# Kernel optimization log

Hardware: AMD Instinct MI355X
Metric: run time of the kernel (lower is better)

## Reference

```python
import jax, jax.numpy as jnp
import numpy as np

K = 20
NEG = 0.2      # leaky relu slope
EPS = 1e-5     # layernorm eps


def knn(x, k=K):
    # x: [B, C, N] -> neighbor indices [B, N, k] by largest negative sq-distance
    xt = jnp.swapaxes(x, 1, 2)                      # [B, N, C]
    inner = -2.0 * jnp.einsum('bnc,bcm->bnm', xt, x)
    xx = jnp.sum(x * x, axis=1)                     # [B, N]
    pd = -xx[:, :, None] - inner - xx[:, None, :]   # [B, N, N]
    _, idx = jax.lax.top_k(pd, k)
    return idx


def graph_feature(x, k=K):
    # x: [B, C, N] -> edge features [B, 2C, N, k] = cat(neighbor - center, center)
    xt = jnp.swapaxes(x, 1, 2)                      # [B, N, C]
    idx = knn(x, k)                                 # [B, N, k]
    nbr = jax.vmap(lambda f, i: f[i])(xt, idx)      # [B, N, k, C]
    ctr = jnp.broadcast_to(xt[:, :, None, :], nbr.shape)
    feat = jnp.concatenate([nbr - ctr, ctr], axis=-1)
    return jnp.transpose(feat, (0, 3, 1, 2))


def lrelu(x):
    return jnp.where(x >= 0, x, NEG * x)


def conv1x1(x, w):
    # x: [B, C, N, k], w: [O, C]  (BatchNorm2d in eval with default stats == identity)
    return jnp.einsum('oc,bcnk->bonk', w, x)


def layernorm(x, g, b):
    m = jnp.mean(x, axis=-1, keepdims=True)
    v = jnp.var(x, axis=-1, keepdims=True)
    return (x - m) * jax.lax.rsqrt(v + EPS) * g + b


def l2n(x):
    return x / jnp.linalg.norm(x, axis=1, keepdims=True)


def fc_layer(x, w, bias, g, beta):
    # l2-normalize -> Linear -> LayerNorm -> LeakyReLU (fc_layer with norm=True, bn=True)
    x = l2n(x)
    x = x @ w.T
    if bias is not None:
        x = x + bias
    return lrelu(layernorm(x, g, beta))


def transform_net(f0, tw1, tw2, tw3, tfc1_w, tfc1_g, tfc1_b, tfc2_w, tfc2_bias, tfc2_g, tfc2_b, tfc3_w, tfc3_b):
    # f0: [B, 6, N, k]
    h = lrelu(conv1x1(f0, tw1))                     # [B, 64, N, k]
    h = lrelu(conv1x1(h, tw2))                      # [B, 128, N, k]
    h = jnp.max(h, axis=-1, keepdims=True)          # [B, 128, N, 1]
    h = lrelu(conv1x1(h, tw3))                      # [B, 1024, N, 1]
    h = jnp.max(h, axis=2)[:, :, 0]                 # [B, 1024]
    h = fc_layer(h, tfc1_w, None, tfc1_g, tfc1_b)   # dgcnn: fc1 bias=False
    h = fc_layer(h, tfc2_w, tfc2_bias, tfc2_g, tfc2_b)
    h = h @ tfc3_w.T + tfc3_b                       # [B, 9]
    h = h + jnp.eye(3, dtype=h.dtype).reshape(9)
    return h.reshape(-1, 3, 3)


def setup_inputs() -> dict:
    key = jax.random.key(0)
    ks = jax.random.split(key, 16)

    def w(k, o, i):
        return jax.random.normal(k, (o, i), dtype=jnp.float32) / np.sqrt(i)

    inp = {
        'x': jax.random.normal(ks[0], (16, 3, 1024), dtype=jnp.float32),
        # transform_net params
        'tw1': w(ks[1], 64, 6),
        'tw2': w(ks[2], 128, 64),
        'tw3': w(ks[3], 1024, 128),
        'tfc1_w': w(ks[4], 512, 1024),
        'tfc1_g': jnp.ones((512,), jnp.float32),
        'tfc1_b': jnp.zeros((512,), jnp.float32),
        'tfc2_w': w(ks[5], 256, 512),
        'tfc2_bias': jnp.zeros((256,), jnp.float32),
        'tfc2_g': jnp.ones((256,), jnp.float32),
        'tfc2_b': jnp.zeros((256,), jnp.float32),
        'tfc3_w': w(ks[6], 9, 256) * 0.01,
        'tfc3_b': jnp.zeros((9,), jnp.float32),
        # EdgeConv params (1x1 convs, bias=False for dgcnn)
        'w1': w(ks[7], 64, 6),
        'w2': w(ks[8], 64, 128),
        'w3': w(ks[9], 128, 128),
        'w4': w(ks[10], 256, 256),
        'w5': w(ks[11], 1024, 512),
    }
    return inp


def reference(x, tw1, tw2, tw3, tfc1_w, tfc1_g, tfc1_b, tfc2_w, tfc2_bias, tfc2_g, tfc2_b,
              tfc3_w, tfc3_b, w1, w2, w3, w4, w5):
    # spatial transform from first graph feature
    f0 = graph_feature(x)                           # [B, 6, N, k]
    t = transform_net(f0, tw1, tw2, tw3, tfc1_w, tfc1_g, tfc1_b,
                      tfc2_w, tfc2_bias, tfc2_g, tfc2_b, tfc3_w, tfc3_b)
    x = jnp.einsum('bij,bjn->bin', t, x)            # [B, 3, N]

    # 4 EdgeConv blocks: graph_feature -> 1x1 conv (+BN identity) -> lrelu -> max over k
    x1 = jnp.max(lrelu(conv1x1(graph_feature(x), w1)), axis=-1)    # [B, 64, N]
    x2 = jnp.max(lrelu(conv1x1(graph_feature(x1), w2)), axis=-1)   # [B, 64, N]
    x3 = jnp.max(lrelu(conv1x1(graph_feature(x2), w3)), axis=-1)   # [B, 128, N]
    x4 = jnp.max(lrelu(conv1x1(graph_feature(x3), w4)), axis=-1)   # [B, 256, N]

    xc = jnp.concatenate([x1, x2, x3, x4], axis=1)  # [B, 512, N]
    x5 = lrelu(jnp.einsum('oc,bcn->bon', w5, xc))   # [B, 1024, N]
    return jnp.max(x5, axis=-1)                     # [B, 1024] global feature
```

## Files before the change

kernel.cpp:

```cpp
#include <hip/hip_runtime.h>
#include <math.h>

#define BATCH 16
#define NPTS 1024
#define KNN 20

__device__ __forceinline__ float lrelu(float v) { return v >= 0.f ? v : 0.2f * v; }

typedef __attribute__((ext_vector_type(8))) short bf16x8;
typedef __attribute__((ext_vector_type(4))) float f32x4;
typedef unsigned long long ull;

__device__ __forceinline__ ushort f2bf(float f) {
  union { float f; unsigned u; } v; v.f = f;
  unsigned r = (v.u + 0x7FFFu + ((v.u >> 16) & 1u)) >> 16;
  return (ushort)r;
}

__device__ __forceinline__ unsigned wave_min_u32(unsigned v) {
  unsigned t;
  t = (unsigned)__builtin_amdgcn_update_dpp((int)v, (int)v, 0x111, 0xf, 0xf, false);
  v = t < v ? t : v;
  t = (unsigned)__builtin_amdgcn_update_dpp((int)v, (int)v, 0x112, 0xf, 0xf, false);
  v = t < v ? t : v;
  t = (unsigned)__builtin_amdgcn_update_dpp((int)v, (int)v, 0x114, 0xf, 0xf, false);
  v = t < v ? t : v;
  t = (unsigned)__builtin_amdgcn_update_dpp((int)v, (int)v, 0x118, 0xf, 0xf, false);
  v = t < v ? t : v;
  t = (unsigned)__builtin_amdgcn_update_dpp((int)v, (int)v, 0x142, 0xf, 0xf, false);
  v = t < v ? t : v;
  t = (unsigned)__builtin_amdgcn_update_dpp((int)v, (int)v, 0x143, 0xf, 0xf, false);
  v = t < v ? t : v;
  return (unsigned)__builtin_amdgcn_readlane((int)v, 63);
}

__global__ __launch_bounds__(256)
void wsplit_t_kernel(const float* __restrict__ W, float* __restrict__ waT,
                     float* __restrict__ wdT, int O, int Cc) {
  int e = blockIdx.x * 256 + threadIdx.x;
  if (e < O * Cc) {
    int c = e / O, o = e - c * O;
    float a = W[o * 2 * Cc + c], bb = W[o * 2 * Cc + Cc + c];
    waT[e] = a; wdT[e] = bb - a;
  }
}

__global__ __launch_bounds__(256)
void wsplit_bf_kernel(const float* __restrict__ W, ushort* __restrict__ wa_bf,
                      ushort* __restrict__ wd_bf, int O, int Cc) {
  int e = blockIdx.x * 256 + threadIdx.x;
  if (e < O * Cc) {
    int o = e / Cc, c = e - o * Cc;
    float a = W[o * 2 * Cc + c], bb = W[o * 2 * Cc + Cc + c];
    wa_bf[e] = f2bf(a); wd_bf[e] = f2bf(bb - a);
  }
}

__global__ __launch_bounds__(256)
void cvt_bf16_kernel(const float* __restrict__ in, ushort* __restrict__ outp, int n) {
  int e = blockIdx.x * 256 + threadIdx.x;
  if (e < n) outp[e] = f2bf(in[e]);
}

__global__ __launch_bounds__(256)
void wtrans_kernel(const float* __restrict__ W, float* __restrict__ wT, int O, int Cc) {
  int e = blockIdx.x * 256 + threadIdx.x;
  if (e < O * Cc) {
    int c = e / O, o = e - c * O;
    wT[e] = W[(size_t)o * Cc + c];
  }
}

__global__ __launch_bounds__(256)
void xx3_kernel(const float* __restrict__ x, float* __restrict__ xx) {
  const int b = blockIdx.y;
  const int n = blockIdx.x * 256 + threadIdx.x;
  const float* xb = x + (size_t)b * 3 * NPTS;
  float a = xb[n], bb = xb[NPTS + n], c = xb[2 * NPTS + n];
  xx[b * NPTS + n] = a * a + bb * bb + c * c;
}

template<int C>
__global__ __launch_bounds__(256)
void knn_cn_kernel(const float* __restrict__ Xt, long sb,
                   const float* __restrict__ xx, int* __restrict__ idxout) {
  __shared__ float sc4[4][NPTS];
  const int b = blockIdx.y, i0 = blockIdx.x * 16;
  const int tid = threadIdx.x;
  const float* Xb = Xt + (size_t)b * sb;
  const int j0 = tid * 4;
  float acc[16][4];
  #pragma unroll
  for (int q = 0; q < 16; ++q)
    #pragma unroll
    for (int u = 0; u < 4; ++u) acc[q][u] = 0.f;
  for (int c = 0; c < C; ++c) {
    const float4 xv = *reinterpret_cast<const float4*>(Xb + (size_t)c * NPTS + j0);
    const float* xr = Xb + (size_t)c * NPTS + i0;
    #pragma unroll
    for (int q = 0; q < 16; ++q) {
      const float xiq = xr[q];
      acc[q][0] = fmaf(xiq, xv.x, acc[q][0]);
      acc[q][1] = fmaf(xiq, xv.y, acc[q][1]);
      acc[q][2] = fmaf(xiq, xv.z, acc[q][2]);
      acc[q][3] = fmaf(xiq, xv.w, acc[q][3]);
    }
  }
  const float4 xxj = *reinterpret_cast<const float4*>(xx + b * NPTS + j0);
  const int wv = tid >> 6, lane = tid & 63;
  unsigned ku[4][16];

  #pragma unroll
  for (int r = 0; r < 4; ++r) {
    if (r > 0) __syncthreads();
    #pragma unroll
    for (int q = 0; q < 4; ++q) {
      const int qq = r * 4 + q;
      float4 st;
      st.x = fmaf(-2.f, acc[qq][0], xxj.x);
      st.y = fmaf(-2.f, acc[qq][1], xxj.y);
      st.z = fmaf(-2.f, acc[qq][2], xxj.z);
      st.w = fmaf(-2.f, acc[qq][3], xxj.w);
      *reinterpret_cast<float4*>(&sc4[q][j0]) = st;
    }
    __syncthreads();
    #pragma unroll
    for (int s = 0; s < 16; ++s) {
      const unsigned u = __float_as_uint(sc4[wv][lane + 64 * s]);
      ku[r][s] = u ^ ((unsigned)((int)u >> 31) | 0x80000000u);
    }
  }

  unsigned c1s[4], c2s[4]; int c1j[4], c2j[4];
  #pragma unroll
  for (int r = 0; r < 4; ++r) {
    unsigned b1 = 0xFFFFFFFFu, b2 = 0xFFFFFFFFu; int s1 = 0, s2 = 0;
    #pragma unroll
    for (int s = 0; s < 16; ++s) {
      const unsigned k = ku[r][s];
      const bool a1 = k < b1, a2 = k < b2;
      const unsigned n1 = a1 ? k : b1;  const int ns1 = a1 ? s : s1;
      const unsigned n2 = a1 ? b1 : (a2 ? k : b2);
      const int ns2 = a1 ? s1 : (a2 ? s : s2);
      b1 = n1; s1 = ns1; b2 = n2; s2 = ns2;
    }
    c1s[r] = b1; c1j[r] = lane + (s1 << 6);
    c2s[r] = b2; c2j[r] = lane + (s2 << 6);
  }
  const unsigned INVS = 0xFFFFFFFFu;
  int my[4] = {0, 0, 0, 0};
  for (int t = 0; t < KNN; ++t) {
    unsigned ws[4]; int wl[4], jw[4];
    #pragma unroll
    for (int r = 0; r < 4; ++r) ws[r] = wave_min_u32(c1s[r]);
    #pragma unroll
    for (int r = 0; r < 4; ++r) wl[r] = __ffsll((long long)__ballot(c1s[r] == ws[r])) - 1;
    #pragma unroll
    for (int r = 0; r < 4; ++r) jw[r] = __builtin_amdgcn_readlane(c1j[r], wl[r]);
    if (lane == t) {
      #pragma unroll
      for (int r = 0; r < 4; ++r) my[r] = jw[r];
    }
    bool cons = false;
    #pragma unroll
    for (int r = 0; r < 4; ++r) {
      const bool win = (lane == wl[r]);
      c1s[r] = win ? c2s[r] : c1s[r];
      c1j[r] = win ? c2j[r] : c1j[r];
      c2s[r] = win ? INVS : c2s[r];
      cons = cons || (c1s[r] == INVS);
    }
    if (__any(cons)) {
      #pragma unroll
      for (int r = 0; r < 4; ++r) {
        if (c1s[r] == INVS) {
          unsigned m1 = INVS, m2 = INVS; int r1 = 0, r2 = 0;
          #pragma unroll
          for (int s = 0; s < 16; ++s) {
            const unsigned k = ku[r][s];
            const bool ok = k > ws[r];
            const bool a1 = ok && (k < m1), a2 = ok && (k < m2);
            const unsigned nm1 = a1 ? k : m1;  const int nr1 = a1 ? s : r1;
            const unsigned nm2 = a1 ? m1 : (a2 ? k : m2);
            const int nr2 = a1 ? r1 : (a2 ? s : r2);
            m1 = nm1; r1 = nr1; m2 = nm2; r2 = nr2;
          }
          c1s[r] = (m1 == INVS) ? 0xFFFFFFFEu : m1;  c1j[r] = lane + (r1 << 6);
          c2s[r] = (m2 == INVS) ? 0xFFFFFFFEu : m2;  c2j[r] = lane + (r2 << 6);
        }
      }
    }
  }
  if (lane < KNN) {
    #pragma unroll
    for (int r = 0; r < 4; ++r)
      idxout[(size_t)(b * NPTS + i0 + r * 4 + wv) * KNN + lane] = my[r];
  }
}

__global__ __launch_bounds__(256)
void gemm_dual_kernel(const float* __restrict__ X, long sxb, int sxn, int sxc,
                      const float* __restrict__ WaT, const float* __restrict__ WdT,
                      int ldW, int C,
                      float* __restrict__ outY, float* __restrict__ outZ,
                      int sob, int son) {
  __shared__ __align__(16) float Xs[16][64];
  __shared__ __align__(16) float Was[16][64];
  __shared__ __align__(16) float Wds[16][64];
  const int b = blockIdx.z;
  const int n0 = blockIdx.x * 64, o0 = blockIdx.y * 64;
  const int tid = threadIdx.x;
  const int lr = tid & 63;
  const int c4 = (tid >> 6) * 4;
  const int tn = tid & 15, to = tid >> 4;
  float accY[4][4], accZ[4][4];
  #pragma unroll
  for (int i = 0; i < 4; ++i)
    #pragma unroll
    for (int j = 0; j < 4; ++j) { accY[i][j] = 0.f; accZ[i][j] = 0.f; }

  const size_t xbase = (size_t)b * sxb;
  for (int k0 = 0; k0 < C; k0 += 16) {
    #pragma unroll
    for (int u = 0; u < 4; ++u) {
      int c = k0 + c4 + u;
      float xv = 0.f, wa = 0.f, wd = 0.f;
      if (c < C) {
        xv = X[xbase + (size_t)(n0 + lr) * sxn + (size_t)c * sxc];
        wa = WaT[(size_t)c * ldW + o0 + lr];
        wd = WdT[(size_t)c * ldW + o0 + lr];
      }
      Xs[c4 + u][lr] = xv;
      Was[c4 + u][lr] = wa;
      Wds[c4 + u][lr] = wd;
    }
    __syncthreads();
    #pragma unroll
    for (int kk = 0; kk < 16; ++kk) {
      const float4 xa = *reinterpret_cast<const float4*>(&Xs[kk][tn * 4]);
      const float4 wav = *reinterpret_cast<const float4*>(&Was[kk][to * 4]);
      const float4 wdv = *reinterpret_cast<const float4*>(&Wds[kk][to * 4]);
      const float xr[4] = {xa.x, xa.y, xa.z, xa.w};
      const float war[4] = {wav.x, wav.y, wav.z, wav.w};
      const float wdr[4] = {wdv.x, wdv.y, wdv.z, wdv.w};
      #pragma unroll
      for (int i = 0; i < 4; ++i)
        #pragma unroll
        for (int j = 0; j < 4; ++j) {
          accY[i][j] = fmaf(xr[i], war[j], accY[i][j]);
          accZ[i][j] = fmaf(xr[i], wdr[j], accZ[i][j]);
        }
    }
    __syncthreads();
  }
  #pragma unroll
  for (int i = 0; i < 4; ++i) {
    const size_t base = (size_t)b * sob + (size_t)(n0 + tn * 4 + i) * son + o0 + to * 4;
    *reinterpret_cast<float4*>(&outY[base]) =
      make_float4(accY[i][0], accY[i][1], accY[i][2], accY[i][3]);
    *reinterpret_cast<float4*>(&outZ[base]) =
      make_float4(accZ[i][0], accZ[i][1], accZ[i][2], accZ[i][3]);
  }
}

template<int EPI>
__global__ __launch_bounds__(256)
void gemm128_kernel(const float* __restrict__ X, long sxb, int scN,
                    const float* __restrict__ WT, int ldW, int C,
                    float* __restrict__ out, int sob, int son, int snb) {
  __shared__ __align__(16) float Xs[16][128];
  __shared__ __align__(16) float Ws[16][128];
  __shared__ __align__(16) float red[16][132];
  const int b = blockIdx.z;
  const int n0 = blockIdx.x * 128, o0 = blockIdx.y * 128;
  const int tid = threadIdx.x;
  const int tn = tid & 15, to = tid >> 4;
  float acc[8][8];
  #pragma unroll
  for (int i = 0; i < 8; ++i)
    #pragma unroll
    for (int j = 0; j < 8; ++j) acc[i][j] = 0.f;

  const size_t xbase = (size_t)b * sxb;
  for (int c0 = 0; c0 < C; c0 += 16) {
    #pragma unroll
    for (int it = 0; it < 2; ++it) {
      const int task = tid + it * 256;
      const int kk = task >> 5, n4 = (task & 31) * 4;
      *reinterpret_cast<float4*>(&Xs[kk][n4]) =
        *reinterpret_cast<const float4*>(&X[xbase + (size_t)(c0 + kk) * scN + n0 + n4]);
      *reinterpret_cast<float4*>(&Ws[kk][n4]) =
        *reinterpret_cast<const float4*>(&WT[(size_t)(c0 + kk) * ldW + o0 + n4]);
    }
    __syncthreads();
    #pragma unroll
    for (int kk = 0; kk < 16; ++kk) {
      const float4 xa0 = *reinterpret_cast<const float4*>(&Xs[kk][tn * 4]);
      const float4 xa1 = *reinterpret_cast<const float4*>(&Xs[kk][64 + tn * 4]);
      const float4 wb0 = *reinterpret_cast<const float4*>(&Ws[kk][to * 4]);
      const float4 wb1 = *reinterpret_cast<const float4*>(&Ws[kk][64 + to * 4]);
      const float xr[8] = {xa0.x, xa0.y, xa0.z, xa0.w, xa1.x, xa1.y, xa1.z, xa1.w};
      const float wr[8] = {wb0.x, wb0.y, wb0.z, wb0.w, wb1.x, wb1.y, wb1.z, wb1.w};
      #pragma unroll
      for (int i = 0; i < 8; ++i)
        #pragma unroll
        for (int j = 0; j < 8; ++j) acc[i][j] = fmaf(xr[i], wr[j], acc[i][j]);
    }
    __syncthreads();
  }

  if (EPI == 0) {
    #pragma unroll
    for (int i = 0; i < 8; ++i) {
      const int n = n0 + (i >> 2) * 64 + tn * 4 + (i & 3);
      float4 s0 = make_float4(acc[i][0], acc[i][1], acc[i][2], acc[i][3]);
      float4 s1 = make_float4(acc[i][4], acc[i][5], acc[i][6], acc[i][7]);
      *reinterpret_cast<float4*>(&out[(size_t)b * sob + (size_t)n * son + o0 + to * 4]) = s0;
      *reinterpret_cast<float4*>(&out[(size_t)b * sob + (size_t)n * son + o0 + 64 + to * 4]) = s1;
    }
  } else {
    #pragma unroll
    for (int j = 0; j < 8; ++j) {
      float m = lrelu(acc[0][j]);
      #pragma unroll
      for (int i = 1; i < 8; ++i) m = fmaxf(m, lrelu(acc[i][j]));
      red[tn][(j >> 2) * 64 + to * 4 + (j & 3)] = m;
    }
    __syncthreads();
    if (tid < 128) {
      float m = red[0][tid];
      #pragma unroll
      for (int t = 1; t < 16; ++t) m = fmaxf(m, red[t][tid]);
      out[(size_t)b * sob + (size_t)blockIdx.x * snb + o0 + tid] = m;
    }
  }
}

template<int EPI>
__global__ __launch_bounds__(256)
void gemm_mfma_kernel(const ushort* __restrict__ Xg, long sxb, int ldX,
                      const ushort* __restrict__ Wg, int ldW, int K,
                      float* __restrict__ out, long sob, int son, int snb) {
  __shared__ __align__(16) ushort As[128 * 64];
  __shared__ __align__(16) ushort Bs[128 * 64];
  __shared__ float red[2][128];
  const int b = blockIdx.z;
  const int n0 = blockIdx.x * 128, o0 = blockIdx.y * 128;
  const int tid = threadIdx.x;
  const int lane = tid & 63;
  const int wrow = (tid >> 6) >> 1, wcol = (tid >> 6) & 1;
  f32x4 acc[4][4];
  #pragma unroll
  for (int i = 0; i < 4; ++i)
    #pragma unroll
    for (int j = 0; j < 4; ++j)
      #pragma unroll
      for (int r = 0; r < 4; ++r) acc[i][j][r] = 0.f;

  const ushort* Xb = Xg + (size_t)b * sxb;
  for (int kb = 0; kb < K; kb += 64) {
    #pragma unroll
    for (int i = 0; i < 4; ++i) {
      const int idx = i * 256 + tid;
      const int n = idx >> 3, kc = idx & 7;
      const bf16x8 xv = *reinterpret_cast<const bf16x8*>(&Xb[(size_t)(n0 + n) * ldX + kb + kc * 8]);
      const bf16x8 wv = *reinterpret_cast<const bf16x8*>(&Wg[(size_t)(o0 + n) * ldW + kb + kc * 8]);
      const int ad = n * 128 + ((kc * 16) ^ ((n & 7) << 4));
      *reinterpret_cast<bf16x8*>((char*)As + ad) = xv;
      *reinterpret_cast<bf16x8*>((char*)Bs + ad) = wv;
    }
    __syncthreads();
    #pragma unroll
    for (int s = 0; s < 2; ++s) {
      bf16x8 af[4], bfr[4];
      const int klane = (s * 64 + ((lane >> 4) << 4));
      #pragma unroll
      for (int f = 0; f < 4; ++f) {
        const int nl = wrow * 64 + f * 16 + (lane & 15);
        af[f] = *reinterpret_cast<const bf16x8*>((char*)As + nl * 128 + (klane ^ ((nl & 7) << 4)));
        const int ol = wcol * 64 + f * 16 + (lane & 15);
        bfr[f] = *reinterpret_cast<const bf16x8*>((char*)Bs + ol * 128 + (klane ^ ((ol & 7) << 4)));
      }
      #pragma unroll
      for (int i = 0; i < 4; ++i)
        #pragma unroll
        for (int j = 0; j < 4; ++j)
          acc[i][j] = __builtin_amdgcn_mfma_f32_16x16x32_bf16(af[i], bfr[j], acc[i][j], 0, 0, 0);
    }
    __syncthreads();
  }

  if (EPI == 0) {
    #pragma unroll
    for (int i = 0; i < 4; ++i)
      #pragma unroll
      for (int r = 0; r < 4; ++r) {
        const int n = n0 + wrow * 64 + i * 16 + ((lane >> 4) << 2) + r;
        #pragma unroll
        for (int j = 0; j < 4; ++j) {
          const int o = o0 + wcol * 64 + j * 16 + (lane & 15);
          out[(size_t)b * sob + (size_t)n * son + o] = acc[i][j][r];
        }
      }
  } else {
    #pragma unroll
    for (int j = 0; j < 4; ++j) {
      float m = -3.4e38f;
      #pragma unroll
      for (int i = 0; i < 4; ++i)
        #pragma unroll
        for (int r = 0; r < 4; ++r) m = fmaxf(m, lrelu(acc[i][j][r]));
      m = fmaxf(m, __shfl_xor(m, 16));
      m = fmaxf(m, __shfl_xor(m, 32));
      if (lane < 16) red[wrow][wcol * 64 + j * 16 + lane] = m;
    }
    __syncthreads();
    if (tid < 128) {
      float m = fmaxf(red[0][tid], red[1][tid]);
      out[(size_t)b * sob + (size_t)blockIdx.x * snb + o0 + tid] = m;
    }
  }
}

template<int O, int TI>
__global__ __launch_bounds__(256)
void edge_max_cn_kernel(const float* __restrict__ y, const float* __restrict__ z,
                        const int* __restrict__ idx, float* __restrict__ outCN,
                        float* __restrict__ xx, ushort* __restrict__ xbf, int choff) {
  __shared__ float tile[TI][O + 1];
  const int b = blockIdx.y;
  const int i0 = blockIdx.x * TI;
  const int wv = threadIdx.x >> 6, lane = threadIdx.x & 63;
  constexpr int OSEG = O / 64;
  constexpr int ROUNDS = TI * OSEG / 4;
  for (int r = 0; r < ROUNDS; ++r) {
    const int item = r * 4 + wv;
    const int il = item / OSEG, os = item - il * OSEG;
    const int i = i0 + il, o = os * 64 + lane;
    const int* ip = idx + (size_t)(b * NPTS + i) * KNN;
    const float zv = z[(size_t)(b * NPTS + i) * O + o];
    float m = -3.4e38f;
    #pragma unroll
    for (int t = 0; t < KNN; ++t) {
      int j = ip[t];
      float v = y[(size_t)(b * NPTS + j) * O + o] + zv;
      m = fmaxf(m, lrelu(v));
    }
    tile[il][o] = m;
    xbf[(size_t)(b * NPTS + i) * 512 + choff + o] = f2bf(m);
  }
  __syncthreads();
  if (xx != nullptr && threadIdx.x < TI) {
    const int il = threadIdx.x;
    float s = 0.f;
    #pragma unroll
    for (int o = 0; o < O; ++o) { float v = tile[il][o]; s = fmaf(v, v, s); }
    xx[b * NPTS + i0 + il] = s;
  }
  for (int e = threadIdx.x; e < TI * O; e += 256) {
    const int o = e / TI, il = e - o * TI;
    outCN[(size_t)b * 512 * NPTS + (size_t)o * NPTS + i0 + il] = tile[il][o];
  }
}

__global__ __launch_bounds__(256)
void h12_gemm_kernel(const float* __restrict__ ya, const float* __restrict__ zb,
                     const int* __restrict__ idx, const float* __restrict__ tw2T,
                     float* __restrict__ h2m) {
  __shared__ __align__(16) float h1s[80][68];
  __shared__ __align__(16) float ws[64][128];
  __shared__ __align__(16) float zbs[4][64];
  __shared__ float ot[128][4];
  __shared__ int idxs[4][KNN];
  const int b = blockIdx.y;
  const int i0 = blockIdx.x * 4;
  const int tid = threadIdx.x;

  #pragma unroll
  for (int it = 0; it < 8; ++it) {
    const int f = tid + it * 256;
    *reinterpret_cast<float4*>(&ws[0][0] + f * 4) =
      *reinterpret_cast<const float4*>(tw2T + (size_t)f * 4);
  }
  if (tid < 64) {
    const int p = tid >> 4, cq = (tid & 15) * 4;
    *reinterpret_cast<float4*>(&zbs[p][cq]) =
      *reinterpret_cast<const float4*>(&zb[(size_t)(b * NPTS + i0 + p) * 64 + cq]);
  }
  if (tid >= 64 && tid < 64 + 4 * KNN) {
    const int e = tid - 64;
    idxs[e / KNN][e % KNN] = idx[(size_t)(b * NPTS + i0) * KNN + e];
  }
  __syncthreads();

  #pragma unroll
  for (int it = 0; it < 5; ++it) {
    const int task = tid + it * 256;
    const int e = task >> 4, cq = (task & 15) * 4;
    const int p = e / KNN, t = e - p * KNN;
    const int j = idxs[p][t];
    const float4 yv = *reinterpret_cast<const float4*>(&ya[(size_t)(b * NPTS + j) * 64 + cq]);
    const float4 zv = *reinterpret_cast<const float4*>(&zbs[p][cq]);
    float4 hv;
    hv.x = lrelu(yv.x + zv.x); hv.y = lrelu(yv.y + zv.y);
    hv.z = lrelu(yv.z + zv.z); hv.w = lrelu(yv.w + zv.w);
    *reinterpret_cast<float4*>(&h1s[e][cq]) = hv;
  }
  __syncthreads();

  const int eg = tid >> 4, og = tid & 15;
  float acc[5][8];
  #pragma unroll
  for (int u = 0; u < 5; ++u)
    #pragma unroll
    for (int v = 0; v < 8; ++v) acc[u][v] = 0.f;
  #pragma unroll 4
  for (int kk = 0; kk < 64; ++kk) {
    float hv[5];
    #pragma unroll
    for (int u = 0; u < 5; ++u) hv[u] = h1s[eg * 5 + u][kk];
    const float4 w0 = *reinterpret_cast<const float4*>(&ws[kk][og * 4]);
    const float4 w1 = *reinterpret_cast<const float4*>(&ws[kk][64 + og * 4]);
    const float wr[8] = {w0.x, w0.y, w0.z, w0.w, w1.x, w1.y, w1.z, w1.w};
    #pragma unroll
    for (int u = 0; u < 5; ++u)
      #pragma unroll
      for (int v = 0; v < 8; ++v) acc[u][v] = fmaf(hv[u], wr[v], acc[u][v]);
  }

  const int p = eg >> 2, d = eg & 3;
  float m[8];
  #pragma unroll
  for (int v = 0; v < 8; ++v) {
    float mm = lrelu(acc[0][v]);
    #pragma unroll
    for (int u = 1; u < 5; ++u) mm = fmaxf(mm, lrelu(acc[u][v]));
    mm = fmaxf(mm, __shfl_xor(mm, 16));
    mm = fmaxf(mm, __shfl_xor(mm, 32));
    m[v] = mm;
  }
  if (d == 0) {
    #pragma unroll
    for (int v = 0; v < 8; ++v) {
      const int o = og * 4 + (v & 3) + (v >> 2) * 64;
      ot[o][p] = m[v];
    }
  }
  __syncthreads();
  if (tid < 128) {
    float4 st = make_float4(ot[tid][0], ot[tid][1], ot[tid][2], ot[tid][3]);
    *reinterpret_cast<float4*>(&h2m[(size_t)(b * 128 + tid) * NPTS + i0]) = st;
  }
}

__global__ __launch_bounds__(256)
void reduce_max_kernel(const float* __restrict__ part, float* __restrict__ outp, int nt) {
  const int b = blockIdx.y;
  const int o = blockIdx.x * 256 + threadIdx.x;
  float m = part[(size_t)(b * nt) * 1024 + o];
  for (int t = 1; t < nt; ++t) m = fmaxf(m, part[(size_t)(b * nt + t) * 1024 + o]);
  outp[b * 1024 + o] = m;
}

__device__ __forceinline__ float block_reduce_sum(float v, float* rbuf) {
  #pragma unroll
  for (int off = 32; off > 0; off >>= 1) v += __shfl_xor(v, off);
  const int w = threadIdx.x >> 6, lane = threadIdx.x & 63;
  const int nw = blockDim.x >> 6;
  if (lane == 0) rbuf[w] = v;
  __syncthreads();
  float tot = 0.f;
  for (int i = 0; i < nw; ++i) tot += rbuf[i];
  __syncthreads();
  return tot;
}

__global__ __launch_bounds__(256)
void fcall_kernel(const float* __restrict__ part,
                  const float* __restrict__ Wt1, const float* __restrict__ g1,
                  const float* __restrict__ bb1,
                  const float* __restrict__ Wt2, const float* __restrict__ bias2,
                  const float* __restrict__ g2, const float* __restrict__ bb2,
                  const float* __restrict__ Wt3, const float* __restrict__ bb3,
                  const float* __restrict__ x, float* __restrict__ xt) {
  __shared__ __align__(16) float gin[1024];
  __shared__ __align__(16) float f1s[512];
  __shared__ float f2s[256];
  __shared__ float hbuf[512];
  __shared__ float rbuf[8];
  __shared__ float tm[9];
  const int b = blockIdx.x, tid = threadIdx.x;
  for (int e = tid; e < 1024; e += 256) {
    const float* pp = part + (size_t)b * 8192 + e;
    float m = pp[0];
    #pragma unroll
    for (int t = 1; t < 8; ++t) m = fmaxf(m, pp[t * 1024]);
    gin[e] = m;
  }
  __syncthreads();
  float ps = 0.f;
  for (int e = tid; e < 1024; e += 256) ps = fmaf(gin[e], gin[e], ps);
  float ss = block_reduce_sum(ps, rbuf);
  float rinv = 1.0f / sqrtf(ss);
  #pragma unroll
  for (int r = 0; r < 2; ++r) {
    int o = tid + r * 256;
    const float* wrow = Wt1 + (size_t)o * 1024;
    float a = 0.f;
    for (int c4 = 0; c4 < 256; ++c4) {
      float4 wv = *reinterpret_cast<const float4*>(wrow + c4 * 4);
      float4 gv = *reinterpret_cast<const float4*>(&gin[c4 * 4]);
      a = fmaf(wv.x, gv.x, a); a = fmaf(wv.y, gv.y, a);
      a = fmaf(wv.z, gv.z, a); a = fmaf(wv.w, gv.w, a);
    }
    hbuf[o] = a * rinv;
  }
  __syncthreads();
  float pm = hbuf[tid] + hbuf[tid + 256];
  float mean = block_reduce_sum(pm, rbuf) * (1.f / 512.f);
  float d0 = hbuf[tid] - mean, d1 = hbuf[tid + 256] - mean;
  float var = block_reduce_sum(d0 * d0 + d1 * d1, rbuf) * (1.f / 512.f);
  float rs = 1.0f / sqrtf(var + 1e-5f);
  #pragma unroll
  for (int r = 0; r < 2; ++r) {
    int o = tid + r * 256;
    f1s[o] = lrelu((hbuf[o] - mean) * rs * g1[o] + bb1[o]);
  }
  __syncthreads();
  float ps2 = 0.f;
  for (int e = tid; e < 512; e += 256) ps2 = fmaf(f1s[e], f1s[e], ps2);
  float ss2 = block_reduce_sum(ps2, rbuf);
  float rinv2 = 1.0f / sqrtf(ss2);
  const float* wrow2 = Wt2 + (size_t)tid * 512;
  float a2 = 0.f;
  for (int c4 = 0; c4 < 128; ++c4) {
    float4 wv = *reinterpret_cast<const float4*>(wrow2 + c4 * 4);
    float4 gv = *reinterpret_cast<const float4*>(&f1s[c4 * 4]);
    a2 = fmaf(wv.x, gv.x, a2); a2 = fmaf(wv.y, gv.y, a2);
    a2 = fmaf(wv.z, gv.z, a2); a2 = fmaf(wv.w, gv.w, a2);
  }
  a2 = a2 * rinv2 + bias2[tid];
  float mean2 = block_reduce_sum(a2, rbuf) * (1.f / 256.f);
  float dd = a2 - mean2;
  float var2 = block_reduce_sum(dd * dd, rbuf) * (1.f / 256.f);
  float rs2 = 1.0f / sqrtf(var2 + 1e-5f);
  f2s[tid] = lrelu((a2 - mean2) * rs2 * g2[tid] + bb2[tid]);
  __syncthreads();
  if (tid < 9) {
    const float* wrow3 = Wt3 + tid * 256;
    float a3 = 0.f;
    for (int c = 0; c < 256; ++c) a3 = fmaf(wrow3[c], f2s[c], a3);
    a3 += bb3[tid];
    if (tid == 0 || tid == 4 || tid == 8) a3 += 1.f;
    tm[tid] = a3;
  }
  __syncthreads();
  const float* xb = x + (size_t)b * 3 * NPTS;
  float* ob = xt + (size_t)b * 3 * NPTS;
  #pragma unroll
  for (int nt = 0; nt < 4; ++nt) {
    const int n = nt * 256 + tid;
    const float x0 = xb[n], x1 = xb[NPTS + n], x2 = xb[2 * NPTS + n];
    #pragma unroll
    for (int i = 0; i < 3; ++i)
      ob[i * NPTS + n] = fmaf(tm[3 * i], x0, fmaf(tm[3 * i + 1], x1, tm[3 * i + 2] * x2));
  }
}

extern "C" void kernel_launch(void* const* d_in, const int* in_sizes, int n_in,
                              void* d_out, int out_size, void* d_ws, size_t ws_size,
                              hipStream_t stream) {
  (void)in_sizes; (void)n_in; (void)out_size; (void)ws_size;
  const float* x       = (const float*)d_in[0];
  const float* tw1     = (const float*)d_in[1];
  const float* tw2     = (const float*)d_in[2];
  const float* tw3     = (const float*)d_in[3];
  const float* tfc1_w  = (const float*)d_in[4];
  const float* tfc1_g  = (const float*)d_in[5];
  const float* tfc1_b  = (const float*)d_in[6];
  const float* tfc2_w  = (const float*)d_in[7];
  const float* tfc2_bias = (const float*)d_in[8];
  const float* tfc2_g  = (const float*)d_in[9];
  const float* tfc2_b  = (const float*)d_in[10];
  const float* tfc3_w  = (const float*)d_in[11];
  const float* tfc3_b  = (const float*)d_in[12];
  const float* w1      = (const float*)d_in[13];
  const float* w2      = (const float*)d_in[14];
  const float* w3      = (const float*)d_in[15];
  const float* w4      = (const float*)d_in[16];
  const float* w5      = (const float*)d_in[17];
  float* out = (float*)d_out;

  char* wsb = (char*)d_ws;
  size_t off = 0;
  auto alloc = [&](size_t bytes) -> void* {
    void* p = wsb + off;
    off += (bytes + 255) & ~(size_t)255;
    return p;
  };
  float* ybuf = (float*)alloc((size_t)BATCH * NPTS * 256 * 4);
  float* zbuf = (float*)alloc((size_t)BATCH * NPTS * 256 * 4);
  float* xcT  = (float*)alloc((size_t)BATCH * 512 * NPTS * 4);
  ushort* xc_bf = (ushort*)alloc((size_t)BATCH * NPTS * 512 * 2);
  float* h2m  = (float*)alloc((size_t)BATCH * 128 * NPTS * 4);
  float* part = (float*)alloc((size_t)BATCH * 16 * 1024 * 4);
  int*   idxb = (int*)alloc((size_t)BATCH * NPTS * KNN * 4);
  float* xxb  = (float*)alloc((size_t)BATCH * NPTS * 4);
  float* xt   = (float*)alloc((size_t)BATCH * 3 * NPTS * 4);
  float* tw1aT = (float*)alloc(3 * 64 * 4);
  float* tw1dT = (float*)alloc(3 * 64 * 4);
  float* w1aT  = (float*)alloc(3 * 64 * 4);
  float* w1dT  = (float*)alloc(3 * 64 * 4);
  float* w2aT  = (float*)alloc(64 * 64 * 4);
  float* w2dT  = (float*)alloc(64 * 64 * 4);
  float* w3aT  = (float*)alloc(64 * 128 * 4);
  float* w3dT  = (float*)alloc(64 * 128 * 4);
  ushort* w4a_bf = (ushort*)alloc(256 * 128 * 2);
  ushort* w4d_bf = (ushort*)alloc(256 * 128 * 2);
  ushort* w5_bf  = (ushort*)alloc(1024 * 512 * 2);
  float* tw2T  = (float*)alloc(64 * 128 * 4);
  float* tw3T  = (float*)alloc(128 * 1024 * 4);

  wsplit_t_kernel<<<1, 256, 0, stream>>>(tw1, tw1aT, tw1dT, 64, 3);
  wsplit_t_kernel<<<1, 256, 0, stream>>>(w1, w1aT, w1dT, 64, 3);
  wsplit_t_kernel<<<16, 256, 0, stream>>>(w2, w2aT, w2dT, 64, 64);
  wsplit_t_kernel<<<32, 256, 0, stream>>>(w3, w3aT, w3dT, 128, 64);
  wsplit_bf_kernel<<<128, 256, 0, stream>>>(w4, w4a_bf, w4d_bf, 256, 128);
  cvt_bf16_kernel<<<2048, 256, 0, stream>>>(w5, w5_bf, 1024 * 512);
  wtrans_kernel<<<32, 256, 0, stream>>>(tw2, tw2T, 128, 64);
  wtrans_kernel<<<512, 256, 0, stream>>>(tw3, tw3T, 1024, 128);

  xx3_kernel<<<dim3(4, 16), 256, 0, stream>>>(x, xxb);
  knn_cn_kernel<3><<<dim3(64, 16), 256, 0, stream>>>(x, 3 * NPTS, xxb, idxb);
  gemm_dual_kernel<<<dim3(16, 1, 16), 256, 0, stream>>>(x, 3 * NPTS, 1, NPTS, tw1aT, tw1dT,
                                                        64, 3, ybuf, zbuf, NPTS * 64, 64);
  h12_gemm_kernel<<<dim3(256, 16), 256, 0, stream>>>(ybuf, zbuf, idxb, tw2T, h2m);
  gemm128_kernel<1><<<dim3(8, 8, 16), 256, 0, stream>>>(h2m, 128 * NPTS, NPTS, tw3T, 1024, 128,
                                                        part, 8 * 1024, 0, 1024);
  fcall_kernel<<<16, 256, 0, stream>>>(part, tfc1_w, tfc1_g, tfc1_b,
                                       tfc2_w, tfc2_bias, tfc2_g, tfc2_b,
                                       tfc3_w, tfc3_b, x, xt);

  xx3_kernel<<<dim3(4, 16), 256, 0, stream>>>(xt, xxb);
  knn_cn_kernel<3><<<dim3(64, 16), 256, 0, stream>>>(xt, 3 * NPTS, xxb, idxb);
  gemm_dual_kernel<<<dim3(16, 1, 16), 256, 0, stream>>>(xt, 3 * NPTS, 1, NPTS, w1aT, w1dT,
                                                        64, 3, ybuf, zbuf, NPTS * 64, 64);
  edge_max_cn_kernel<64, 64><<<dim3(16, 16), 256, 0, stream>>>(ybuf, zbuf, idxb, xcT, xxb,
                                                               xc_bf, 0);

  knn_cn_kernel<64><<<dim3(64, 16), 256, 0, stream>>>(xcT, 512 * NPTS, xxb, idxb);
  gemm_dual_kernel<<<dim3(16, 1, 16), 256, 0, stream>>>(xcT, 512 * NPTS, 1, NPTS, w2aT, w2dT,
                                                        64, 64, ybuf, zbuf, NPTS * 64, 64);
  edge_max_cn_kernel<64, 64><<<dim3(16, 16), 256, 0, stream>>>(ybuf, zbuf, idxb,
                                                               xcT + 64 * NPTS, xxb, xc_bf, 64);

  knn_cn_kernel<64><<<dim3(64, 16), 256, 0, stream>>>(xcT + 64 * NPTS, 512 * NPTS, xxb, idxb);
  gemm_dual_kernel<<<dim3(16, 2, 16), 256, 0, stream>>>(xcT + 64 * NPTS, 512 * NPTS, 1, NPTS,
                                                        w3aT, w3dT, 128, 64,
                                                        ybuf, zbuf, NPTS * 128, 128);
  edge_max_cn_kernel<128, 64><<<dim3(16, 16), 256, 0, stream>>>(ybuf, zbuf, idxb,
                                                                xcT + 128 * NPTS, xxb, xc_bf, 128);

  knn_cn_kernel<128><<<dim3(64, 16), 256, 0, stream>>>(xcT + 128 * NPTS, 512 * NPTS, xxb, idxb);
  gemm_mfma_kernel<0><<<dim3(8, 2, 16), 256, 0, stream>>>(xc_bf + 128, (long)NPTS * 512, 512,
                                                          w4a_bf, 128, 128,
                                                          ybuf, (long)NPTS * 256, 256, 0);
  gemm_mfma_kernel<0><<<dim3(8, 2, 16), 256, 0, stream>>>(xc_bf + 128, (long)NPTS * 512, 512,
                                                          w4d_bf, 128, 128,
                                                          zbuf, (long)NPTS * 256, 256, 0);
  edge_max_cn_kernel<256, 32><<<dim3(32, 16), 256, 0, stream>>>(ybuf, zbuf, idxb,
                                                                xcT + 256 * NPTS, nullptr,
                                                                xc_bf, 256);

  gemm_mfma_kernel<1><<<dim3(8, 8, 16), 256, 0, stream>>>(xc_bf, (long)NPTS * 512, 512,
                                                          w5_bf, 512, 512,
                                                          part, 8 * 1024, 0, 1024);
  reduce_max_kernel<<<dim3(4, 16), 256, 0, stream>>>(part, out, 8);
}
```

Before: 734.9 us.

## Merge weight-prep kernels, split FC head into batched kernels, simplify knn argmin

Eight weight-preparation launches are folded into one flat-indexed prep kernel to cut launch overhead. The single per-batch FC head kernel, which streamed the full FC1/FC2 weight matrices once per batch, is split into three kernels. FC1 and FC2 now tile the weights in shared memory and reuse each tile across all 16 batches, and a final per-batch kernel does the last layernorm, the 3x3 transform and the point rotation. In the knn top-k loop, the ballot/ffs/readlane winner lookup is replaced by a second DPP wave-min over candidate indices, which changes tie-breaking to the smallest index. The FC split adds two launches and intermediate global buffers.

```diff
diff --git a/kernel.cpp b/kernel.cpp
--- a/kernel.cpp
+++ b/kernel.cpp
@@ -9,7 +9,6 @@
 
 typedef __attribute__((ext_vector_type(8))) short bf16x8;
 typedef __attribute__((ext_vector_type(4))) float f32x4;
-typedef unsigned long long ull;
 
 __device__ __forceinline__ ushort f2bf(float f) {
   union { float f; unsigned u; } v; v.f = f;
@@ -35,39 +34,56 @@
 }
 
 __global__ __launch_bounds__(256)
-void wsplit_t_kernel(const float* __restrict__ W, float* __restrict__ waT,
-                     float* __restrict__ wdT, int O, int Cc) {
-  int e = blockIdx.x * 256 + threadIdx.x;
-  if (e < O * Cc) {
-    int c = e / O, o = e - c * O;
-    float a = W[o * 2 * Cc + c], bb = W[o * 2 * Cc + Cc + c];
-    waT[e] = a; wdT[e] = bb - a;
-  }
-}
-
-__global__ __launch_bounds__(256)
-void wsplit_bf_kernel(const float* __restrict__ W, ushort* __restrict__ wa_bf,
-                      ushort* __restrict__ wd_bf, int O, int Cc) {
-  int e = blockIdx.x * 256 + threadIdx.x;
-  if (e < O * Cc) {
-    int o = e / Cc, c = e - o * Cc;
-    float a = W[o * 2 * Cc + c], bb = W[o * 2 * Cc + Cc + c];
-    wa_bf[e] = f2bf(a); wd_bf[e] = f2bf(bb - a);
-  }
-}
-
-__global__ __launch_bounds__(256)
-void cvt_bf16_kernel(const float* __restrict__ in, ushort* __restrict__ outp, int n) {
-  int e = blockIdx.x * 256 + threadIdx.x;
-  if (e < n) outp[e] = f2bf(in[e]);
-}
-
-__global__ __launch_bounds__(256)
-void wtrans_kernel(const float* __restrict__ W, float* __restrict__ wT, int O, int Cc) {
-  int e = blockIdx.x * 256 + threadIdx.x;
-  if (e < O * Cc) {
-    int c = e / O, o = e - c * O;
-    wT[e] = W[(size_t)o * Cc + c];
+void prep_all_kernel(const float* __restrict__ tw1, const float* __restrict__ w1,
+                     const float* __restrict__ w2, const float* __restrict__ w3,
+                     const float* __restrict__ w4, const float* __restrict__ w5,
+                     const float* __restrict__ tw2, const float* __restrict__ tw3,
+                     float* __restrict__ tw1aT, float* __restrict__ tw1dT,
+                     float* __restrict__ w1aT, float* __restrict__ w1dT,
+                     float* __restrict__ w2aT, float* __restrict__ w2dT,
+                     float* __restrict__ w3aT, float* __restrict__ w3dT,
+                     ushort* __restrict__ w4a_bf, ushort* __restrict__ w4d_bf,
+                     ushort* __restrict__ w5_bf,
+                     float* __restrict__ tw2T, float* __restrict__ tw3T) {
+  int g = blockIdx.x * 256 + threadIdx.x;
+  if (g < 524288) { w5_bf[g] = f2bf(w5[g]); return; }
+  g -= 524288;
+  if (g < 131072) { int c = g >> 10, o = g & 1023; tw3T[g] = tw3[o * 128 + c]; return; }
+  g -= 131072;
+  if (g < 32768) {
+    int o = g >> 7, c = g & 127;
+    float a = w4[o * 256 + c], bb = w4[o * 256 + 128 + c];
+    w4a_bf[g] = f2bf(a); w4d_bf[g] = f2bf(bb - a);
+    return;
+  }
+  g -= 32768;
+  if (g < 8192) {
+    int c = g >> 7, o = g & 127;
+    float a = w3[o * 128 + c], bb = w3[o * 128 + 64 + c];
+    w3aT[g] = a; w3dT[g] = bb - a;
+    return;
+  }
+  g -= 8192;
+  if (g < 8192) { int c = g >> 7, o = g & 127; tw2T[g] = tw2[o * 64 + c]; return; }
+  g -= 8192;
+  if (g < 4096) {
+    int c = g >> 6, o = g & 63;
+    float a = w2[o * 128 + c], bb = w2[o * 128 + 64 + c];
+    w2aT[g] = a; w2dT[g] = bb - a;
+    return;
+  }
+  g -= 4096;
+  if (g < 192) {
+    int c = g >> 6, o = g & 63;
+    float a = tw1[o * 6 + c], bb = tw1[o * 6 + 3 + c];
+    tw1aT[g] = a; tw1dT[g] = bb - a;
+    return;
+  }
+  g -= 192;
+  if (g < 192) {
+    int c = g >> 6, o = g & 63;
+    float a = w1[o * 6 + c], bb = w1[o * 6 + 3 + c];
+    w1aT[g] = a; w1dT[g] = bb - a;
   }
 }
 
@@ -131,7 +147,7 @@
     }
   }
 
-  unsigned c1s[4], c2s[4]; int c1j[4], c2j[4];
+  unsigned c1s[4], c2s[4]; unsigned c1j[4], c2j[4];
   #pragma unroll
   for (int r = 0; r < 4; ++r) {
     unsigned b1 = 0xFFFFFFFFu, b2 = 0xFFFFFFFFu; int s1 = 0, s2 = 0;
@@ -144,27 +160,28 @@
       const int ns2 = a1 ? s1 : (a2 ? s : s2);
       b1 = n1; s1 = ns1; b2 = n2; s2 = ns2;
     }
-    c1s[r] = b1; c1j[r] = lane + (s1 << 6);
-    c2s[r] = b2; c2j[r] = lane + (s2 << 6);
+    c1s[r] = b1; c1j[r] = (unsigned)(lane + (s1 << 6));
+    c2s[r] = b2; c2j[r] = (unsigned)(lane + (s2 << 6));
   }
   const unsigned INVS = 0xFFFFFFFFu;
   int my[4] = {0, 0, 0, 0};
   for (int t = 0; t < KNN; ++t) {
-    unsigned ws[4]; int wl[4], jw[4];
+    unsigned ws[4], jw[4];
     #pragma unroll
     for (int r = 0; r < 4; ++r) ws[r] = wave_min_u32(c1s[r]);
     #pragma unroll
-    for (int r = 0; r < 4; ++r) wl[r] = __ffsll((long long)__ballot(c1s[r] == ws[r])) - 1;
-    #pragma unroll
-    for (int r = 0; r < 4; ++r) jw[r] = __builtin_amdgcn_readlane(c1j[r], wl[r]);
+    for (int r = 0; r < 4; ++r) {
+      const unsigned jc = (c1s[r] == ws[r]) ? c1j[r] : 0xFFFFFFFFu;
+      jw[r] = wave_min_u32(jc);
+    }
     if (lane == t) {
       #pragma unroll
-      for (int r = 0; r < 4; ++r) my[r] = jw[r];
+      for (int r = 0; r < 4; ++r) my[r] = (int)jw[r];
     }
     bool cons = false;
     #pragma unroll
     for (int r = 0; r < 4; ++r) {
-      const bool win = (lane == wl[r]);
+      const bool win = (c1s[r] == ws[r]) && (c1j[r] == jw[r]);
       c1s[r] = win ? c2s[r] : c1s[r];
       c1j[r] = win ? c2j[r] : c1j[r];
       c2s[r] = win ? INVS : c2s[r];
@@ -185,8 +202,8 @@
             const int nr2 = a1 ? r1 : (a2 ? s : r2);
             m1 = nm1; r1 = nr1; m2 = nm2; r2 = nr2;
           }
-          c1s[r] = (m1 == INVS) ? 0xFFFFFFFEu : m1;  c1j[r] = lane + (r1 << 6);
-          c2s[r] = (m2 == INVS) ? 0xFFFFFFFEu : m2;  c2j[r] = lane + (r2 << 6);
+          c1s[r] = (m1 == INVS) ? 0xFFFFFFFEu : m1;  c1j[r] = (unsigned)(lane + (r1 << 6));
+          c2s[r] = (m2 == INVS) ? 0xFFFFFFFEu : m2;  c2j[r] = (unsigned)(lane + (r2 << 6));
         }
       }
     }
@@ -576,80 +593,135 @@
 }
 
 __global__ __launch_bounds__(256)
-void fcall_kernel(const float* __restrict__ part,
-                  const float* __restrict__ Wt1, const float* __restrict__ g1,
-                  const float* __restrict__ bb1,
-                  const float* __restrict__ Wt2, const float* __restrict__ bias2,
-                  const float* __restrict__ g2, const float* __restrict__ bb2,
-                  const float* __restrict__ Wt3, const float* __restrict__ bb3,
-                  const float* __restrict__ x, float* __restrict__ xt) {
-  __shared__ __align__(16) float gin[1024];
-  __shared__ __align__(16) float f1s[512];
+void fc1g_kernel(const float* __restrict__ part, const float* __restrict__ Wt1,
+                 float* __restrict__ h1g) {
+  __shared__ __align__(16) float gin[16][1024];
+  __shared__ __align__(16) float Ws[64][65];
+  __shared__ float rbuf[8];
+  __shared__ float rinvs[16];
+  const int tid = threadIdx.x;
+  const int o0 = blockIdx.x * 64;
+  for (int e = tid; e < 16 * 1024; e += 256) {
+    const int b = e >> 10, i = e & 1023;
+    const float* pp = part + (size_t)b * 8192 + i;
+    float m = pp[0];
+    #pragma unroll
+    for (int t = 1; t < 8; ++t) m = fmaxf(m, pp[t * 1024]);
+    gin[b][i] = m;
+  }
+  __syncthreads();
+  for (int b = 0; b < 16; ++b) {
+    float ps = 0.f;
+    for (int e = tid; e < 1024; e += 256) ps = fmaf(gin[b][e], gin[b][e], ps);
+    float ss = block_reduce_sum(ps, rbuf);
+    if (tid == 0) rinvs[b] = 1.0f / sqrtf(ss);
+  }
+  __syncthreads();
+  const int o = tid & 63, bg = tid >> 6;
+  float acc[4] = {0.f, 0.f, 0.f, 0.f};
+  for (int k0 = 0; k0 < 1024; k0 += 64) {
+    __syncthreads();
+    for (int t4 = tid; t4 < 64 * 16; t4 += 256) {
+      const int oo = t4 >> 4, kq = t4 & 15;
+      const float4 wv = *reinterpret_cast<const float4*>(
+          &Wt1[(size_t)(o0 + oo) * 1024 + k0 + kq * 4]);
+      Ws[oo][kq * 4 + 0] = wv.x; Ws[oo][kq * 4 + 1] = wv.y;
+      Ws[oo][kq * 4 + 2] = wv.z; Ws[oo][kq * 4 + 3] = wv.w;
+    }
+    __syncthreads();
+    #pragma unroll 16
+    for (int kk = 0; kk < 64; ++kk) {
+      const float w = Ws[o][kk];
+      #pragma unroll
+      for (int u = 0; u < 4; ++u)
+        acc[u] = fmaf(w, gin[bg * 4 + u][k0 + kk], acc[u]);
+    }
+  }
+  #pragma unroll
+  for (int u = 0; u < 4; ++u) {
+    const int b = bg * 4 + u;
+    h1g[b * 512 + o0 + o] = acc[u] * rinvs[b];
+  }
+}
+
+__global__ __launch_bounds__(256)
+void fc2g_kernel(const float* __restrict__ h1g, const float* __restrict__ g1,
+                 const float* __restrict__ bb1, const float* __restrict__ Wt2,
+                 const float* __restrict__ bias2, float* __restrict__ h2g) {
+  __shared__ __align__(16) float f1s[16][512];
+  __shared__ __align__(16) float Ws[64][65];
+  __shared__ float rbuf[8];
+  __shared__ float rinv2s[16];
+  const int tid = threadIdx.x;
+  const int o0 = blockIdx.x * 64;
+  for (int e = tid; e < 16 * 512; e += 256) {
+    const int b = e >> 9, i = e & 511;
+    f1s[b][i] = h1g[b * 512 + i];
+  }
+  __syncthreads();
+  for (int b = 0; b < 16; ++b) {
+    float ps = 0.f;
+    for (int e = tid; e < 512; e += 256) ps += f1s[b][e];
+    float mean = block_reduce_sum(ps, rbuf) * (1.f / 512.f);
+    float vs = 0.f;
+    for (int e = tid; e < 512; e += 256) { float d = f1s[b][e] - mean; vs = fmaf(d, d, vs); }
+    float var = block_reduce_sum(vs, rbuf) * (1.f / 512.f);
+    float rs = 1.0f / sqrtf(var + 1e-5f);
+    for (int e = tid; e < 512; e += 256)
+      f1s[b][e] = lrelu((f1s[b][e] - mean) * rs * g1[e] + bb1[e]);
+    float ps2 = 0.f;
+    for (int e = tid; e < 512; e += 256) ps2 = fmaf(f1s[b][e], f1s[b][e], ps2);
+    float ss2 = block_reduce_sum(ps2, rbuf);
+    if (tid == 0) rinv2s[b] = 1.0f / sqrtf(ss2);
+  }
+  __syncthreads();
+  const int o = tid & 63, bg = tid >> 6;
+  float acc[4] = {0.f, 0.f, 0.f, 0.f};
+  for (int k0 = 0; k0 < 512; k0 += 64) {
+    __syncthreads();
+    for (int t4 = tid; t4 < 64 * 16; t4 += 256) {
+      const int oo = t4 >> 4, kq = t4 & 15;
+      const float4 wv = *reinterpret_cast<const float4*>(
+          &Wt2[(size_t)(o0 + oo) * 512 + k0 + kq * 4]);
+      Ws[oo][kq * 4 + 0] = wv.x; Ws[oo][kq * 4 + 1] = wv.y;
+      Ws[oo][kq * 4 + 2] = wv.z; Ws[oo][kq * 4 + 3] = wv.w;
+    }
+    __syncthreads();
+    #pragma unroll 16
+    for (int kk = 0; kk < 64; ++kk) {
+      const float w = Ws[o][kk];
+      #pragma unroll
+      for (int u = 0; u < 4; ++u)
+        acc[u] = fmaf(w, f1s[bg * 4 + u][k0 + kk], acc[u]);
+    }
+  }
+  #pragma unroll
+  for (int u = 0; u < 4; ++u) {
+    const int b = bg * 4 + u;
+    h2g[b * 256 + o0 + o] = acc[u] * rinv2s[b] + bias2[o0 + o];
+  }
+}
+
+__global__ __launch_bounds__(256)
+void fc3x_kernel(const float* __restrict__ h2g, const float* __restrict__ g2,
+                 const float* __restrict__ bb2, const float* __restrict__ Wt3,
+                 const float* __restrict__ bb3, const float* __restrict__ x,
+                 float* __restrict__ xt) {
   __shared__ float f2s[256];
-  __shared__ float hbuf[512];
   __shared__ float rbuf[8];
   __shared__ float tm[9];
   const int b = blockIdx.x, tid = threadIdx.x;
-  for (int e = tid; e < 1024; e += 256) {
-    const float* pp = part + (size_t)b * 8192 + e;
-    float m = pp[0];
-    #pragma unroll
-    for (int t = 1; t < 8; ++t) m = fmaxf(m, pp[t * 1024]);
-    gin[e] = m;
-  }
-  __syncthreads();
-  float ps = 0.f;
-  for (int e = tid; e < 1024; e += 256) ps = fmaf(gin[e], gin[e], ps);
-  float ss = block_reduce_sum(ps, rbuf);
-  float rinv = 1.0f / sqrtf(ss);
-  #pragma unroll
-  for (int r = 0; r < 2; ++r) {
-    int o = tid + r * 256;
-    const float* wrow = Wt1 + (size_t)o * 1024;
-    float a = 0.f;
-    for (int c4 = 0; c4 < 256; ++c4) {
-      float4 wv = *reinterpret_cast<const float4*>(wrow + c4 * 4);
-      float4 gv = *reinterpret_cast<const float4*>(&gin[c4 * 4]);
-      a = fmaf(wv.x, gv.x, a); a = fmaf(wv.y, gv.y, a);
-      a = fmaf(wv.z, gv.z, a); a = fmaf(wv.w, gv.w, a);
-    }
-    hbuf[o] = a * rinv;
-  }
-  __syncthreads();
-  float pm = hbuf[tid] + hbuf[tid + 256];
-  float mean = block_reduce_sum(pm, rbuf) * (1.f / 512.f);
-  float d0 = hbuf[tid] - mean, d1 = hbuf[tid + 256] - mean;
-  float var = block_reduce_sum(d0 * d0 + d1 * d1, rbuf) * (1.f / 512.f);
+  const float a2 = h2g[b * 256 + tid];
+  float mean = block_reduce_sum(a2, rbuf) * (1.f / 256.f);
+  float d = a2 - mean;
+  float var = block_reduce_sum(d * d, rbuf) * (1.f / 256.f);
   float rs = 1.0f / sqrtf(var + 1e-5f);
-  #pragma unroll
-  for (int r = 0; r < 2; ++r) {
-    int o = tid + r * 256;
-    f1s[o] = lrelu((hbuf[o] - mean) * rs * g1[o] + bb1[o]);
-  }
-  __syncthreads();
-  float ps2 = 0.f;
-  for (int e = tid; e < 512; e += 256) ps2 = fmaf(f1s[e], f1s[e], ps2);
-  float ss2 = block_reduce_sum(ps2, rbuf);
-  float rinv2 = 1.0f / sqrtf(ss2);
-  const float* wrow2 = Wt2 + (size_t)tid * 512;
-  float a2 = 0.f;
-  for (int c4 = 0; c4 < 128; ++c4) {
-    float4 wv = *reinterpret_cast<const float4*>(wrow2 + c4 * 4);
-    float4 gv = *reinterpret_cast<const float4*>(&f1s[c4 * 4]);
-    a2 = fmaf(wv.x, gv.x, a2); a2 = fmaf(wv.y, gv.y, a2);
-    a2 = fmaf(wv.z, gv.z, a2); a2 = fmaf(wv.w, gv.w, a2);
-  }
-  a2 = a2 * rinv2 + bias2[tid];
-  float mean2 = block_reduce_sum(a2, rbuf) * (1.f / 256.f);
-  float dd = a2 - mean2;
-  float var2 = block_reduce_sum(dd * dd, rbuf) * (1.f / 256.f);
-  float rs2 = 1.0f / sqrtf(var2 + 1e-5f);
-  f2s[tid] = lrelu((a2 - mean2) * rs2 * g2[tid] + bb2[tid]);
+  f2s[tid] = lrelu((a2 - mean) * rs * g2[tid] + bb2[tid]);
   __syncthreads();
   if (tid < 9) {
-    const float* wrow3 = Wt3 + tid * 256;
+    const float* wrow = Wt3 + tid * 256;
     float a3 = 0.f;
-    for (int c = 0; c < 256; ++c) a3 = fmaf(wrow3[c], f2s[c], a3);
+    for (int c = 0; c < 256; ++c) a3 = fmaf(wrow[c], f2s[c], a3);
     a3 += bb3[tid];
     if (tid == 0 || tid == 4 || tid == 8) a3 += 1.f;
     tm[tid] = a3;
@@ -707,6 +779,8 @@
   int*   idxb = (int*)alloc((size_t)BATCH * NPTS * KNN * 4);
   float* xxb  = (float*)alloc((size_t)BATCH * NPTS * 4);
   float* xt   = (float*)alloc((size_t)BATCH * 3 * NPTS * 4);
+  float* h1g  = (float*)alloc((size_t)BATCH * 512 * 4);
+  float* h2g  = (float*)alloc((size_t)BATCH * 256 * 4);
   float* tw1aT = (float*)alloc(3 * 64 * 4);
   float* tw1dT = (float*)alloc(3 * 64 * 4);
   float* w1aT  = (float*)alloc(3 * 64 * 4);
@@ -721,14 +795,10 @@
   float* tw2T  = (float*)alloc(64 * 128 * 4);
   float* tw3T  = (float*)alloc(128 * 1024 * 4);
 
-  wsplit_t_kernel<<<1, 256, 0, stream>>>(tw1, tw1aT, tw1dT, 64, 3);
-  wsplit_t_kernel<<<1, 256, 0, stream>>>(w1, w1aT, w1dT, 64, 3);
-  wsplit_t_kernel<<<16, 256, 0, stream>>>(w2, w2aT, w2dT, 64, 64);
-  wsplit_t_kernel<<<32, 256, 0, stream>>>(w3, w3aT, w3dT, 128, 64);
-  wsplit_bf_kernel<<<128, 256, 0, stream>>>(w4, w4a_bf, w4d_bf, 256, 128);
-  cvt_bf16_kernel<<<2048, 256, 0, stream>>>(w5, w5_bf, 1024 * 512);
-  wtrans_kernel<<<32, 256, 0, stream>>>(tw2, tw2T, 128, 64);
-  wtrans_kernel<<<512, 256, 0, stream>>>(tw3, tw3T, 1024, 128);
+  prep_all_kernel<<<2770, 256, 0, stream>>>(tw1, w1, w2, w3, w4, w5, tw2, tw3,
+                                            tw1aT, tw1dT, w1aT, w1dT, w2aT, w2dT,
+                                            w3aT, w3dT, w4a_bf, w4d_bf, w5_bf,
+                                            tw2T, tw3T);
 
   xx3_kernel<<<dim3(4, 16), 256, 0, stream>>>(x, xxb);
   knn_cn_kernel<3><<<dim3(64, 16), 256, 0, stream>>>(x, 3 * NPTS, xxb, idxb);
@@ -737,9 +807,9 @@
   h12_gemm_kernel<<<dim3(256, 16), 256, 0, stream>>>(ybuf, zbuf, idxb, tw2T, h2m);
   gemm128_kernel<1><<<dim3(8, 8, 16), 256, 0, stream>>>(h2m, 128 * NPTS, NPTS, tw3T, 1024, 128,
                                                         part, 8 * 1024, 0, 1024);
-  fcall_kernel<<<16, 256, 0, stream>>>(part, tfc1_w, tfc1_g, tfc1_b,
-                                       tfc2_w, tfc2_bias, tfc2_g, tfc2_b,
-                                       tfc3_w, tfc3_b, x, xt);
+  fc1g_kernel<<<8, 256, 0, stream>>>(part, tfc1_w, h1g);
+  fc2g_kernel<<<4, 256, 0, stream>>>(h1g, tfc1_g, tfc1_b, tfc2_w, tfc2_bias, h2g);
+  fc3x_kernel<<<16, 256, 0, stream>>>(h2g, tfc2_g, tfc2_b, tfc3_w, tfc3_b, x, xt);
 
   xx3_kernel<<<dim3(4, 16), 256, 0, stream>>>(xt, xxb);
   knn_cn_kernel<3><<<dim3(64, 16), 256, 0, stream>>>(xt, 3 * NPTS, xxb, idxb);
```

Result: slower. 814.4 us (+10.8%).
